# Performance work log

Measured on AMD Instinct MI355X. Metric: run time of the kernel, lower is better.

Reference implementation:

```python
import jax, jax.numpy as jnp
import numpy as np
from jax import lax

SEQ, IN, H, NC, L = 2048, 1024, 1024, 512, 3


def _lstm_layer(x_seq, W_ih, W_hh, b_ih, b_hh):
    # x_seq: [T, in] -> hs: [T, H]. PyTorch gate order: i, f, g, o.
    Hd = W_hh.shape[1]
    # Precompute input contribution for all timesteps (one big GEMM).
    gx = x_seq @ W_ih.T + (b_ih + b_hh)  # [T, 4H]

    def step(carry, gx_t):
        h, c = carry
        gates = gx_t + h @ W_hh.T  # [4H]
        i, f, g, o = jnp.split(gates, 4)
        i = jax.nn.sigmoid(i)
        f = jax.nn.sigmoid(f)
        g = jnp.tanh(g)
        o = jax.nn.sigmoid(o)
        c = f * c + i * g
        h = o * jnp.tanh(c)
        return (h, c), h

    h0 = jnp.zeros((Hd,), x_seq.dtype)
    c0 = jnp.zeros((Hd,), x_seq.dtype)
    _, hs = lax.scan(step, (h0, c0), gx)
    return hs


def setup_inputs() -> dict:
    key = jax.random.key(0)
    ks = jax.random.split(key, 16)
    s = 1.0 / np.sqrt(H)  # PyTorch LSTM init scale
    d = {"x": jax.random.normal(ks[0], (SEQ, IN), jnp.float32)}
    i = 1
    for l in range(L):
        in_dim = IN if l == 0 else H
        d[f"W_ih_{l}"] = jax.random.normal(ks[i], (4 * H, in_dim), jnp.float32) * s; i += 1
        d[f"W_hh_{l}"] = jax.random.normal(ks[i], (4 * H, H), jnp.float32) * s; i += 1
        d[f"b_ih_{l}"] = jax.random.normal(ks[i], (4 * H,), jnp.float32) * s; i += 1
        d[f"b_hh_{l}"] = jax.random.normal(ks[i], (4 * H,), jnp.float32) * s; i += 1
    d["fc_w"] = jax.random.normal(ks[13], (NC, H), jnp.float32) * s
    d["fc_b"] = jax.random.normal(ks[14], (NC,), jnp.float32) * s
    return d


def reference(x, W_ih_0, W_hh_0, b_ih_0, b_hh_0,
              W_ih_1, W_hh_1, b_ih_1, b_hh_1,
              W_ih_2, W_hh_2, b_ih_2, b_hh_2,
              fc_w, fc_b):
    h = _lstm_layer(x, W_ih_0, W_hh_0, b_ih_0, b_hh_0)
    h = _lstm_layer(h, W_ih_1, W_hh_1, b_ih_1, b_hh_1)
    h = _lstm_layer(h, W_ih_2, W_hh_2, b_ih_2, b_hh_2)
    return h @ fc_w.T + fc_b  # [SEQ, NC]
```

## Files before the change

kernel.cpp:

```cpp
#include <hip/hip_runtime.h>

#define HDIM  1024
#define FOURH 4096
#define TSEQ  2048
#define NCLS  512

#define SCANB  64
#define GEMMB  32
#define U16    16
#define DRING  128
#define GXRING 128
#define CHUNK  64
#define NCHUNK 32

#define CNT0 0
#define CNT1 64
#define CD0  128
#define CD1  192
#define SP1  256
#define SP2  320
#define SYNC_BYTES 2048
#define HDR_BYTES 32768

union SharedU {
    struct { float h[HDIM]; float gate[4][U16]; } scan;
    struct { float As[16][72]; float Bs[16][132]; } gemm;
};

__device__ __forceinline__ unsigned long long ald(const unsigned long long* p) {
    return __hip_atomic_load(p, __ATOMIC_RELAXED, __HIP_MEMORY_SCOPE_AGENT);
}
__device__ __forceinline__ void ast(unsigned long long* p, unsigned long long v) {
    __hip_atomic_store(p, v, __ATOMIC_RELAXED, __HIP_MEMORY_SCOPE_AGENT);
}
__device__ __forceinline__ unsigned ald32(const unsigned* p) {
    return __hip_atomic_load(p, __ATOMIC_RELAXED, __HIP_MEMORY_SCOPE_AGENT);
}
__device__ __forceinline__ void ast32(unsigned* p, unsigned v) {
    __hip_atomic_store(p, v, __ATOMIC_RELAXED, __HIP_MEMORY_SCOPE_AGENT);
}

__device__ __forceinline__ float fsig(float x)  { return 1.f / (1.f + __expf(-x)); }
__device__ __forceinline__ float ftanh(float x) { return 1.f - 2.f / (1.f + __expf(2.f * x)); }

__global__ __launch_bounds__(256) void gemm_bias_kernel(
    const float* __restrict__ A, const float* __restrict__ B,
    const float* __restrict__ bias1, const float* __restrict__ bias2,
    float* __restrict__ C, int M, int N, int K)
{
    __shared__ float As[16][68];
    __shared__ float Bs[16][68];

    const int tid = threadIdx.x;
    const int tx = tid & 15;
    const int ty = tid >> 4;
    const int n0 = blockIdx.x * 64;
    const int m0 = blockIdx.y * 64;
    const int r  = tid >> 2;
    const int kq = tid & 3;

    float acc[4][4];
#pragma unroll
    for (int i = 0; i < 4; ++i)
#pragma unroll
        for (int j = 0; j < 4; ++j) acc[i][j] = 0.f;

    for (int k0 = 0; k0 < K; k0 += 16) {
        float4 va = *(const float4*)&A[(size_t)(m0 + r) * K + k0 + 4 * kq];
        float4 vb = *(const float4*)&B[(size_t)(n0 + r) * K + k0 + 4 * kq];
        As[4 * kq + 0][r] = va.x; As[4 * kq + 1][r] = va.y;
        As[4 * kq + 2][r] = va.z; As[4 * kq + 3][r] = va.w;
        Bs[4 * kq + 0][r] = vb.x; Bs[4 * kq + 1][r] = vb.y;
        Bs[4 * kq + 2][r] = vb.z; Bs[4 * kq + 3][r] = vb.w;
        __syncthreads();
#pragma unroll
        for (int kk = 0; kk < 16; ++kk) {
            float4 a = *(const float4*)&As[kk][4 * ty];
            float4 b = *(const float4*)&Bs[kk][4 * tx];
            acc[0][0] = fmaf(a.x, b.x, acc[0][0]);
            acc[0][1] = fmaf(a.x, b.y, acc[0][1]);
            acc[0][2] = fmaf(a.x, b.z, acc[0][2]);
            acc[0][3] = fmaf(a.x, b.w, acc[0][3]);
            acc[1][0] = fmaf(a.y, b.x, acc[1][0]);
            acc[1][1] = fmaf(a.y, b.y, acc[1][1]);
            acc[1][2] = fmaf(a.y, b.z, acc[1][2]);
            acc[1][3] = fmaf(a.y, b.w, acc[1][3]);
            acc[2][0] = fmaf(a.z, b.x, acc[2][0]);
            acc[2][1] = fmaf(a.z, b.y, acc[2][1]);
            acc[2][2] = fmaf(a.z, b.z, acc[2][2]);
            acc[2][3] = fmaf(a.z, b.w, acc[2][3]);
            acc[3][0] = fmaf(a.w, b.x, acc[3][0]);
            acc[3][1] = fmaf(a.w, b.y, acc[3][1]);
            acc[3][2] = fmaf(a.w, b.z, acc[3][2]);
            acc[3][3] = fmaf(a.w, b.w, acc[3][3]);
        }
        __syncthreads();
    }

    float4 bv = *(const float4*)&bias1[n0 + 4 * tx];
    if (bias2) {
        float4 b2 = *(const float4*)&bias2[n0 + 4 * tx];
        bv.x += b2.x; bv.y += b2.y; bv.z += b2.z; bv.w += b2.w;
    }
#pragma unroll
    for (int i = 0; i < 4; ++i) {
        const int row = m0 + 4 * ty + i;
        float4 o;
        o.x = acc[i][0] + bv.x;
        o.y = acc[i][1] + bv.y;
        o.z = acc[i][2] + bv.z;
        o.w = acc[i][3] + bv.w;
        *(float4*)&C[(size_t)row * N + n0 + 4 * tx] = o;
    }
}

#define LOAD_GX(T) do { if (lane < 32) {                                      \
    const int g_ = lane >> 3, up_ = lane & 7;                                 \
    const unsigned long long pk_ = ald(gxb +                                  \
        (((size_t)((T) & gxmask)) * FOURH + g_ * HDIM + u0 + 2 * up_) / 2);   \
    gxlo = __uint_as_float((unsigned)pk_);                                    \
    gxhi = __uint_as_float((unsigned)(pk_ >> 32)); } } while (0)

__device__ void scan_role(int bi,
    const float* __restrict__ Whh,
    const unsigned long long* __restrict__ gxb, unsigned gxmask,
    unsigned long long* __restrict__ ring,
    const unsigned* cdSrc,
    const unsigned* cdBp,
    unsigned* sp,
    float* __restrict__ h2,
    SharedU* sm, unsigned* qflag)
{
    const int tid  = threadIdx.x;
    const int w    = tid >> 6;
    const int lane = tid & 63;
    const int g    = w & 3;
    const int ub   = (w >> 2) * 8;
    const int u0   = bi * U16;

    float4 wv[8][4];
#pragma unroll
    for (int u = 0; u < 8; ++u) {
        const float* Wr = Whh + (size_t)(g * HDIM + u0 + ub + u) * HDIM;
#pragma unroll
        for (int j = 0; j < 4; ++j)
            wv[u][j] = *(const float4*)(Wr + 256 * j + 4 * lane);
    }
    { float2 z = {0.f, 0.f}; *(float2*)(sm->scan.h + 2 * tid) = z; }
    if (tid < 4) qflag[tid] = 0u;
    float cst = 0.f;
    float gxlo = 0.f, gxhi = 0.f;
    __syncthreads();

    for (int t = 0; t < TSEQ; ++t) {
        if (w == 7) {
            if ((t & (CHUNK - 1)) == 0) {
                if (cdSrc && lane == 0) {
                    const unsigned need = (unsigned)(t >> 6) + 1u;
                    while (ald32(cdSrc) < need) __builtin_amdgcn_s_sleep(4);
                }
                LOAD_GX(t);
            }
            if (cdBp && t >= DRING && lane == 0) {
                const unsigned need = (unsigned)((t - DRING) >> 6) + 1u;
                while (ald32(cdBp) < need) __builtin_amdgcn_s_sleep(4);
            }
        }

        float acc[8];
#pragma unroll
        for (int u = 0; u < 8; ++u) acc[u] = 0.f;
#pragma unroll
        for (int j = 0; j < 4; ++j) {
            if (t) {
                const unsigned need = 2u * (unsigned)t;
                while (__hip_atomic_load(qflag + j, __ATOMIC_RELAXED,
                                         __HIP_MEMORY_SCOPE_WORKGROUP) < need) {}
                asm volatile("s_waitcnt lgkmcnt(0)" ::: "memory");
                __builtin_amdgcn_sched_barrier(0);
            }
            const float4 hvj = *(const float4*)(sm->scan.h + 256 * j + 4 * lane);
#pragma unroll
            for (int u = 0; u < 8; ++u) {
                acc[u] = fmaf(wv[u][j].x, hvj.x, acc[u]);
                acc[u] = fmaf(wv[u][j].y, hvj.y, acc[u]);
                acc[u] = fmaf(wv[u][j].z, hvj.z, acc[u]);
                acc[u] = fmaf(wv[u][j].w, hvj.w, acc[u]);
            }
        }
#pragma unroll
        for (int off = 32; off; off >>= 1)
#pragma unroll
            for (int u = 0; u < 8; ++u)
                acc[u] += __shfl_xor(acc[u], off, 64);
        if (lane == 0)
#pragma unroll
            for (int u = 0; u < 8; ++u) sm->scan.gate[g][ub + u] = acc[u];
        __syncthreads();

        const unsigned tag = (unsigned)(t + 1);
        if (w == 7) {
            const int src = (lane & 15) >> 1;
            float gv[4];
#pragma unroll
            for (int gg = 0; gg < 4; ++gg) {
                const float a = __shfl(gxlo, 8 * gg + src, 64);
                const float b = __shfl(gxhi, 8 * gg + src, 64);
                gv[gg] = (lane & 1) ? b : a;
            }
            if (lane < U16) {
                const float gi = sm->scan.gate[0][lane] + gv[0];
                const float gf = sm->scan.gate[1][lane] + gv[1];
                const float gg_ = sm->scan.gate[2][lane] + gv[2];
                const float go = sm->scan.gate[3][lane] + gv[3];
                const float si = fsig(gi);
                const float sf = fsig(gf);
                const float tg = ftanh(gg_);
                const float so = fsig(go);
                cst = sf * cst + si * tg;
                const float h = so * ftanh(cst);
                ast(ring + (size_t)(t & (DRING - 1)) * HDIM + u0 + lane,
                    ((unsigned long long)tag << 32) |
                    (unsigned long long)__float_as_uint(h));
                if (h2) h2[(size_t)t * HDIM + u0 + lane] = h;
            }
            if (sp && bi == 0 && lane == 0) ast32(sp, (unsigned)t);
            if (((t + 1) & (CHUNK - 1)) != 0 && t + 1 < TSEQ) LOAD_GX(t + 1);
        }

        if (t + 1 < TSEQ) {
            const unsigned long long* hb = ring + (size_t)(t & (DRING - 1)) * HDIM;
            unsigned long long v0 = 0, v1 = 0;
            bool got0 = false, got1 = false;
            while (!(got0 && got1)) {
                if (!got0) {
                    const unsigned long long x = ald(hb + 2 * tid);
                    if ((unsigned)(x >> 32) == tag) { v0 = x; got0 = true; }
                }
                if (!got1) {
                    const unsigned long long x = ald(hb + 2 * tid + 1);
                    if ((unsigned)(x >> 32) == tag) { v1 = x; got1 = true; }
                }
                if (!(got0 && got1)) __builtin_amdgcn_s_sleep(1);
            }
            sm->scan.h[2 * tid]     = __uint_as_float((unsigned)v0);
            sm->scan.h[2 * tid + 1] = __uint_as_float((unsigned)v1);
            asm volatile("s_waitcnt lgkmcnt(0)" ::: "memory");
            if (lane == 0)
                __hip_atomic_fetch_add(qflag + (w >> 1), 1u, __ATOMIC_RELAXED,
                                       __HIP_MEMORY_SCOPE_WORKGROUP);
        }
    }
}

__device__ void gemm_role(int tix,
    const unsigned long long* __restrict__ ringS,
    const float* __restrict__ Wih,
    const float* __restrict__ bih, const float* __restrict__ bhh,
    float* __restrict__ gxr,
    unsigned* cnt, unsigned* cd, const unsigned* spC,
    SharedU* sm)
{
    const int tid = threadIdx.x;
    const int tx = tid & 31, ty = tid >> 5;
    const int n0 = tix * 128;
    const int tt = tid >> 3, ke = tid & 7;
    const int cB = tid >> 2, kq = tid & 3;

    float4 bv;
    {
        const float4 b1 = *(const float4*)(bih + n0 + 4 * tx);
        const float4 b2 = *(const float4*)(bhh + n0 + 4 * tx);
        bv.x = b1.x + b2.x; bv.y = b1.y + b2.y;
        bv.z = b1.z + b2.z; bv.w = b1.w + b2.w;
    }
    unsigned long long* gxr64 = (unsigned long long*)gxr;

    for (int q = 0; q < NCHUNK; ++q) {
        if (q >= GXRING / CHUNK && tid == 0) {
            const unsigned need = (unsigned)((q - GXRING / CHUNK + 1) * CHUNK + 2);
            while (ald32(spC) < need) __builtin_amdgcn_s_sleep(8);
        }
        __syncthreads();

        float acc[4][4];
#pragma unroll
        for (int i = 0; i < 4; ++i)
#pragma unroll
            for (int j = 0; j < 4; ++j) acc[i][j] = 0.f;

        for (int k0 = 0; k0 < HDIM; k0 += 16) {
            {
                const int trow = q * CHUNK + tt;
                const unsigned expt = (unsigned)(trow + 1);
                const unsigned long long* srcp =
                    ringS + (size_t)(trow & (DRING - 1)) * HDIM + k0 + 2 * ke;
#pragma unroll
                for (int e = 0; e < 2; ++e) {
                    unsigned long long x;
                    while ((unsigned)((x = ald(srcp + e)) >> 32) != expt)
                        __builtin_amdgcn_s_sleep(1);
                    sm->gemm.As[2 * ke + e][tt] = __uint_as_float((unsigned)x);
                }
            }
            {
                const float4 vb = *(const float4*)(Wih + (size_t)(n0 + cB) * HDIM + k0 + 4 * kq);
                sm->gemm.Bs[4 * kq + 0][cB] = vb.x;
                sm->gemm.Bs[4 * kq + 1][cB] = vb.y;
                sm->gemm.Bs[4 * kq + 2][cB] = vb.z;
                sm->gemm.Bs[4 * kq + 3][cB] = vb.w;
            }
            __syncthreads();
#pragma unroll
            for (int kk = 0; kk < 16; ++kk) {
                const float4 a = *(const float4*)&sm->gemm.As[kk][4 * ty];
                const float4 b = *(const float4*)&sm->gemm.Bs[kk][4 * tx];
                acc[0][0] = fmaf(a.x, b.x, acc[0][0]);
                acc[0][1] = fmaf(a.x, b.y, acc[0][1]);
                acc[0][2] = fmaf(a.x, b.z, acc[0][2]);
                acc[0][3] = fmaf(a.x, b.w, acc[0][3]);
                acc[1][0] = fmaf(a.y, b.x, acc[1][0]);
                acc[1][1] = fmaf(a.y, b.y, acc[1][1]);
                acc[1][2] = fmaf(a.y, b.z, acc[1][2]);
                acc[1][3] = fmaf(a.y, b.w, acc[1][3]);
                acc[2][0] = fmaf(a.z, b.x, acc[2][0]);
                acc[2][1] = fmaf(a.z, b.y, acc[2][1]);
                acc[2][2] = fmaf(a.z, b.z, acc[2][2]);
                acc[2][3] = fmaf(a.z, b.w, acc[2][3]);
                acc[3][0] = fmaf(a.w, b.x, acc[3][0]);
                acc[3][1] = fmaf(a.w, b.y, acc[3][1]);
                acc[3][2] = fmaf(a.w, b.z, acc[3][2]);
                acc[3][3] = fmaf(a.w, b.w, acc[3][3]);
            }
            __syncthreads();
        }

#pragma unroll
        for (int i = 0; i < 4; ++i) {
            const int trow = q * CHUNK + 4 * ty + i;
            const float o0 = acc[i][0] + bv.x;
            const float o1 = acc[i][1] + bv.y;
            const float o2 = acc[i][2] + bv.z;
            const float o3 = acc[i][3] + bv.w;
            const size_t base =
                ((size_t)(trow & (GXRING - 1)) * FOURH + n0 + 4 * tx) / 2;
            ast(gxr64 + base,
                ((unsigned long long)__float_as_uint(o1) << 32) | __float_as_uint(o0));
            ast(gxr64 + base + 1,
                ((unsigned long long)__float_as_uint(o3) << 32) | __float_as_uint(o2));
        }
        asm volatile("s_waitcnt vmcnt(0)" ::: "memory");
        __syncthreads();
        if (tid == 0) {
            const unsigned old = __hip_atomic_fetch_add(cnt + q, 1u,
                                     __ATOMIC_RELAXED, __HIP_MEMORY_SCOPE_AGENT);
            if (old + 1u == (unsigned)GEMMB) ast32(cd, (unsigned)(q + 1));
        }
    }
}

__global__ __launch_bounds__(512) void fused_scan(
    const float* __restrict__ gx0,
    const float* __restrict__ Whh0, const float* __restrict__ Whh1,
    const float* __restrict__ Whh2,
    const float* __restrict__ Wih1, const float* __restrict__ Wih2,
    const float* __restrict__ bih1, const float* __restrict__ bhh1,
    const float* __restrict__ bih2, const float* __restrict__ bhh2,
    unsigned long long* ring0, unsigned long long* ring1, unsigned long long* ring2,
    float* gxr1, float* gxr2,
    float* h2out, unsigned* syncw)
{
    __shared__ SharedU sm;
    __shared__ unsigned qflag[4];
    const int lb = blockIdx.x;
    if (lb < 3 * SCANB) {
        const int layer = lb >> 6;
        const int bi    = lb & 63;
        if (layer == 0)
            scan_role(bi, Whh0, (const unsigned long long*)gx0, 2047u, ring0,
                      nullptr, syncw + CD0, nullptr, nullptr, &sm, qflag);
        else if (layer == 1)
            scan_role(bi, Whh1, (const unsigned long long*)gxr1, GXRING - 1u, ring1,
                      syncw + CD0, syncw + CD1, syncw + SP1, nullptr, &sm, qflag);
        else
            scan_role(bi, Whh2, (const unsigned long long*)gxr2, GXRING - 1u, ring2,
                      syncw + CD1, nullptr, syncw + SP2, h2out, &sm, qflag);
    } else {
        const int gb  = lb - 3 * SCANB;
        const int gl  = gb >> 5;
        const int tix = gb & 31;
        if (gl == 0)
            gemm_role(tix, ring0, Wih1, bih1, bhh1, gxr1,
                      syncw + CNT0, syncw + CD0, syncw + SP1, &sm);
        else
            gemm_role(tix, ring1, Wih2, bih2, bhh2, gxr2,
                      syncw + CNT1, syncw + CD1, syncw + SP2, &sm);
    }
}

extern "C" void kernel_launch(void* const* d_in, const int* in_sizes, int n_in,
                              void* d_out, int out_size, void* d_ws, size_t ws_size,
                              hipStream_t stream)
{
    (void)in_sizes; (void)n_in; (void)out_size; (void)ws_size;

    const float* x = (const float*)d_in[0];
    const float* W_ih[3] = {(const float*)d_in[1], (const float*)d_in[5], (const float*)d_in[9]};
    const float* W_hh[3] = {(const float*)d_in[2], (const float*)d_in[6], (const float*)d_in[10]};
    const float* b_ih[3] = {(const float*)d_in[3], (const float*)d_in[7], (const float*)d_in[11]};
    const float* b_hh[3] = {(const float*)d_in[4], (const float*)d_in[8], (const float*)d_in[12]};
    const float* fc_w = (const float*)d_in[13];
    const float* fc_b = (const float*)d_in[14];
    float* out = (float*)d_out;

    unsigned* syncw = (unsigned*)d_ws;
    float* gx = (float*)((char*)d_ws + HDR_BYTES);
    float* A  = gx + (size_t)TSEQ * FOURH;
    unsigned long long* ring0 = (unsigned long long*)(A + (size_t)TSEQ * HDIM);
    unsigned long long* ring1 = ring0 + (size_t)DRING * HDIM;
    unsigned long long* ring2 = ring1 + (size_t)DRING * HDIM;
    float* gxr1 = (float*)(ring2 + (size_t)DRING * HDIM);
    float* gxr2 = gxr1 + (size_t)GXRING * FOURH;

    hipMemsetAsync(syncw, 0, SYNC_BYTES, stream);

    {
        dim3 g(FOURH / 64, TSEQ / 64);
        gemm_bias_kernel<<<g, 256, 0, stream>>>(x, W_ih[0], b_ih[0], b_hh[0],
                                                gx, TSEQ, FOURH, HDIM);
    }

    {
        const float* gx0_c = gx;
        float* h2 = A;
        void* args[] = {
            (void*)&gx0_c,
            (void*)&W_hh[0], (void*)&W_hh[1], (void*)&W_hh[2],
            (void*)&W_ih[1], (void*)&W_ih[2],
            (void*)&b_ih[1], (void*)&b_hh[1],
            (void*)&b_ih[2], (void*)&b_hh[2],
            (void*)&ring0, (void*)&ring1, (void*)&ring2,
            (void*)&gxr1, (void*)&gxr2,
            (void*)&h2, (void*)&syncw
        };
        hipLaunchCooperativeKernel((void*)fused_scan,
                                   dim3(3 * SCANB + 2 * GEMMB), dim3(512),
                                   args, 0, stream);
    }

    {
        dim3 g(NCLS / 64, TSEQ / 64);
        gemm_bias_kernel<<<g, 256, 0, stream>>>(A, fc_w, fc_b, nullptr,
                                                out, TSEQ, NCLS, HDIM);
    }
}
```

Measured before the change: 8.066 ms.

## Distribute LSTM cell update across all waves and drop per-step block barrier

Each wave now owns two hidden units across all four gates, so the gate reduction and the cell update happen inside the wave instead of going through shared memory to a single wave. The per-step __syncthreads is replaced by a workgroup-scope atomic counter that guards the overwrite of shared h. The dot products use packed two-wide FMAs. This shortens the serial critical path of each recurrent step, at the cost of more complex shuffle reductions and a hand-built memory-ordering scheme that is delicate to get right.

```diff
diff --git a/kernel.cpp b/kernel.cpp
--- a/kernel.cpp
+++ b/kernel.cpp
@@ -22,8 +22,10 @@
 #define SYNC_BYTES 2048
 #define HDR_BYTES 32768
 
+typedef float v2f __attribute__((ext_vector_type(2)));
+
 union SharedU {
-    struct { float h[HDIM]; float gate[4][U16]; } scan;
+    struct { float h[HDIM]; } scan;
     struct { float As[16][72]; float Bs[16][132]; } gemm;
 };
 
@@ -114,12 +116,10 @@
     }
 }
 
-#define LOAD_GX(T) do { if (lane < 32) {                                      \
-    const int g_ = lane >> 3, up_ = lane & 7;                                 \
-    const unsigned long long pk_ = ald(gxb +                                  \
-        (((size_t)((T) & gxmask)) * FOURH + g_ * HDIM + u0 + 2 * up_) / 2);   \
-    gxlo = __uint_as_float((unsigned)pk_);                                    \
-    gxhi = __uint_as_float((unsigned)(pk_ >> 32)); } } while (0)
+#define LOAD_GXS(T) do { if (lane < 8) {                                      \
+    gxs = __uint_as_float(ald32((const unsigned*)gxb +                        \
+        (size_t)((T) & gxmask) * FOURH + (size_t)(lane >> 1) * HDIM           \
+        + u0 + 2 * w + (lane & 1))); } } while (0)
 
 __device__ void scan_role(int bi,
     const float* __restrict__ Whh,
@@ -129,47 +129,57 @@
     const unsigned* cdBp,
     unsigned* sp,
     float* __restrict__ h2,
-    SharedU* sm, unsigned* qflag)
+    SharedU* sm, unsigned* qflag, unsigned* rall)
 {
     const int tid  = threadIdx.x;
     const int w    = tid >> 6;
     const int lane = tid & 63;
-    const int g    = w & 3;
-    const int ub   = (w >> 2) * 8;
+    const int uu   = lane & 1;
     const int u0   = bi * U16;
 
-    float4 wv[8][4];
-#pragma unroll
-    for (int u = 0; u < 8; ++u) {
-        const float* Wr = Whh + (size_t)(g * HDIM + u0 + ub + u) * HDIM;
-#pragma unroll
-        for (int j = 0; j < 4; ++j)
-            wv[u][j] = *(const float4*)(Wr + 256 * j + 4 * lane);
+    v2f wv[8][8];
+#pragma unroll
+    for (int rg = 0; rg < 8; ++rg) {
+        const float* Wr = Whh +
+            (size_t)((rg >> 1) * HDIM + u0 + 2 * w + (rg & 1)) * HDIM;
+#pragma unroll
+        for (int j = 0; j < 4; ++j) {
+            const float4 q = *(const float4*)(Wr + 256 * j + 4 * lane);
+            v2f qa = {q.x, q.y}, qb = {q.z, q.w};
+            wv[rg][2 * j]     = qa;
+            wv[rg][2 * j + 1] = qb;
+        }
     }
     { float2 z = {0.f, 0.f}; *(float2*)(sm->scan.h + 2 * tid) = z; }
     if (tid < 4) qflag[tid] = 0u;
+    if (tid == 0) *rall = 0u;
     float cst = 0.f;
-    float gxlo = 0.f, gxhi = 0.f;
+    float gxs = 0.f;
+    unsigned cdc = 0u, bpc = 0u;
     __syncthreads();
 
     for (int t = 0; t < TSEQ; ++t) {
-        if (w == 7) {
-            if ((t & (CHUNK - 1)) == 0) {
-                if (cdSrc && lane == 0) {
-                    const unsigned need = (unsigned)(t >> 6) + 1u;
-                    while (ald32(cdSrc) < need) __builtin_amdgcn_s_sleep(4);
+        if (cdBp && t >= DRING && lane == 0) {
+            const unsigned need = (unsigned)((t - DRING) >> 6) + 1u;
+            while (bpc < need) {
+                bpc = ald32(cdBp);
+                if (bpc < need) __builtin_amdgcn_s_sleep(4);
+            }
+        }
+        if ((t & (CHUNK - 1)) == 0) {
+            if (cdSrc && lane == 0) {
+                const unsigned need = (unsigned)(t >> 6) + 1u;
+                while (cdc < need) {
+                    cdc = ald32(cdSrc);
+                    if (cdc < need) __builtin_amdgcn_s_sleep(4);
                 }
-                LOAD_GX(t);
-            }
-            if (cdBp && t >= DRING && lane == 0) {
-                const unsigned need = (unsigned)((t - DRING) >> 6) + 1u;
-                while (ald32(cdBp) < need) __builtin_amdgcn_s_sleep(4);
-            }
-        }
-
-        float acc[8];
-#pragma unroll
-        for (int u = 0; u < 8; ++u) acc[u] = 0.f;
+            }
+            LOAD_GXS(t);
+        }
+
+        v2f acc2[8];
+#pragma unroll
+        for (int rg = 0; rg < 8; ++rg) { v2f z = {0.f, 0.f}; acc2[rg] = z; }
 #pragma unroll
         for (int j = 0; j < 4; ++j) {
             if (t) {
@@ -179,54 +189,66 @@
                 asm volatile("s_waitcnt lgkmcnt(0)" ::: "memory");
                 __builtin_amdgcn_sched_barrier(0);
             }
-            const float4 hvj = *(const float4*)(sm->scan.h + 256 * j + 4 * lane);
-#pragma unroll
-            for (int u = 0; u < 8; ++u) {
-                acc[u] = fmaf(wv[u][j].x, hvj.x, acc[u]);
-                acc[u] = fmaf(wv[u][j].y, hvj.y, acc[u]);
-                acc[u] = fmaf(wv[u][j].z, hvj.z, acc[u]);
-                acc[u] = fmaf(wv[u][j].w, hvj.w, acc[u]);
-            }
-        }
-#pragma unroll
-        for (int off = 32; off; off >>= 1)
-#pragma unroll
-            for (int u = 0; u < 8; ++u)
-                acc[u] += __shfl_xor(acc[u], off, 64);
+            const float4 hq = *(const float4*)(sm->scan.h + 256 * j + 4 * lane);
+            const v2f hA = {hq.x, hq.y};
+            const v2f hB = {hq.z, hq.w};
+#pragma unroll
+            for (int rg = 0; rg < 8; ++rg) {
+                acc2[rg] = __builtin_elementwise_fma(wv[rg][2 * j],     hA, acc2[rg]);
+                acc2[rg] = __builtin_elementwise_fma(wv[rg][2 * j + 1], hB, acc2[rg]);
+            }
+        }
+        float a[8];
+#pragma unroll
+        for (int rg = 0; rg < 8; ++rg) a[rg] = acc2[rg].x + acc2[rg].y;
+
+        asm volatile("" ::: "memory");
         if (lane == 0)
-#pragma unroll
-            for (int u = 0; u < 8; ++u) sm->scan.gate[g][ub + u] = acc[u];
-        __syncthreads();
-
+            __hip_atomic_fetch_add(rall, 1u, __ATOMIC_RELAXED,
+                                   __HIP_MEMORY_SCOPE_WORKGROUP);
+
+#pragma unroll
+        for (int off = 1; off <= 4; off <<= 1)
+#pragma unroll
+            for (int rg = 0; rg < 8; ++rg)
+                a[rg] += __shfl_xor(a[rg], off, 64);
+        const int l7 = lane & 7;
+        const float s0 = (l7 & 1) ? a[1] : a[0];
+        const float s1 = (l7 & 1) ? a[3] : a[2];
+        const float s2 = (l7 & 1) ? a[5] : a[4];
+        const float s3 = (l7 & 1) ? a[7] : a[6];
+        const float t0 = (l7 & 2) ? s1 : s0;
+        const float t1 = (l7 & 2) ? s3 : s2;
+        float x = (l7 & 4) ? t1 : t0;
+        x += __shfl_xor(x, 8, 64);
+        x += __shfl_xor(x, 16, 64);
+        x += __shfl_xor(x, 32, 64);
+
+        float gsum[4], gxv[4];
+#pragma unroll
+        for (int g = 0; g < 4; ++g) {
+            gsum[g] = __shfl(x,   2 * g + uu, 64);
+            gxv[g]  = __shfl(gxs, 2 * g + uu, 64);
+        }
         const unsigned tag = (unsigned)(t + 1);
-        if (w == 7) {
-            const int src = (lane & 15) >> 1;
-            float gv[4];
-#pragma unroll
-            for (int gg = 0; gg < 4; ++gg) {
-                const float a = __shfl(gxlo, 8 * gg + src, 64);
-                const float b = __shfl(gxhi, 8 * gg + src, 64);
-                gv[gg] = (lane & 1) ? b : a;
-            }
-            if (lane < U16) {
-                const float gi = sm->scan.gate[0][lane] + gv[0];
-                const float gf = sm->scan.gate[1][lane] + gv[1];
-                const float gg_ = sm->scan.gate[2][lane] + gv[2];
-                const float go = sm->scan.gate[3][lane] + gv[3];
-                const float si = fsig(gi);
-                const float sf = fsig(gf);
-                const float tg = ftanh(gg_);
-                const float so = fsig(go);
-                cst = sf * cst + si * tg;
-                const float h = so * ftanh(cst);
-                ast(ring + (size_t)(t & (DRING - 1)) * HDIM + u0 + lane,
+        {
+            const float gi = gsum[0] + gxv[0];
+            const float gf = gsum[1] + gxv[1];
+            const float gg = gsum[2] + gxv[2];
+            const float go = gsum[3] + gxv[3];
+            const float si = fsig(gi), sf = fsig(gf);
+            const float tg = ftanh(gg), so = fsig(go);
+            cst = sf * cst + si * tg;
+            const float hval = so * ftanh(cst);
+            if (lane < 2) {
+                if (h2) h2[(size_t)t * HDIM + u0 + 2 * w + lane] = hval;
+                ast(ring + (size_t)(t & (DRING - 1)) * HDIM + u0 + 2 * w + lane,
                     ((unsigned long long)tag << 32) |
-                    (unsigned long long)__float_as_uint(h));
-                if (h2) h2[(size_t)t * HDIM + u0 + lane] = h;
-            }
-            if (sp && bi == 0 && lane == 0) ast32(sp, (unsigned)t);
-            if (((t + 1) & (CHUNK - 1)) != 0 && t + 1 < TSEQ) LOAD_GX(t + 1);
-        }
+                    (unsigned long long)__float_as_uint(hval));
+            }
+        }
+        if (sp && bi == 0 && w == 0 && lane == 0) ast32(sp, (unsigned)t);
+        if (((t + 1) & (CHUNK - 1)) != 0 && t + 1 < TSEQ) LOAD_GXS(t + 1);
 
         if (t + 1 < TSEQ) {
             const unsigned long long* hb = ring + (size_t)(t & (DRING - 1)) * HDIM;
@@ -234,18 +256,24 @@
             bool got0 = false, got1 = false;
             while (!(got0 && got1)) {
                 if (!got0) {
-                    const unsigned long long x = ald(hb + 2 * tid);
-                    if ((unsigned)(x >> 32) == tag) { v0 = x; got0 = true; }
+                    const unsigned long long y = ald(hb + 2 * tid);
+                    if ((unsigned)(y >> 32) == tag) { v0 = y; got0 = true; }
                 }
                 if (!got1) {
-                    const unsigned long long x = ald(hb + 2 * tid + 1);
-                    if ((unsigned)(x >> 32) == tag) { v1 = x; got1 = true; }
+                    const unsigned long long y = ald(hb + 2 * tid + 1);
+                    if ((unsigned)(y >> 32) == tag) { v1 = y; got1 = true; }
                 }
                 if (!(got0 && got1)) __builtin_amdgcn_s_sleep(1);
             }
+            const unsigned needR = 8u * (unsigned)(t + 1);
+            while (__hip_atomic_load(rall, __ATOMIC_RELAXED,
+                                     __HIP_MEMORY_SCOPE_WORKGROUP) < needR) {}
+            asm volatile("s_waitcnt lgkmcnt(0)" ::: "memory");
+            __builtin_amdgcn_sched_barrier(0);
             sm->scan.h[2 * tid]     = __uint_as_float((unsigned)v0);
             sm->scan.h[2 * tid + 1] = __uint_as_float((unsigned)v1);
             asm volatile("s_waitcnt lgkmcnt(0)" ::: "memory");
+            __builtin_amdgcn_sched_barrier(0);
             if (lane == 0)
                 __hip_atomic_fetch_add(qflag + (w >> 1), 1u, __ATOMIC_RELAXED,
                                        __HIP_MEMORY_SCOPE_WORKGROUP);
@@ -372,19 +400,20 @@
 {
     __shared__ SharedU sm;
     __shared__ unsigned qflag[4];
+    __shared__ unsigned rall;
     const int lb = blockIdx.x;
     if (lb < 3 * SCANB) {
         const int layer = lb >> 6;
         const int bi    = lb & 63;
         if (layer == 0)
             scan_role(bi, Whh0, (const unsigned long long*)gx0, 2047u, ring0,
-                      nullptr, syncw + CD0, nullptr, nullptr, &sm, qflag);
+                      nullptr, syncw + CD0, nullptr, nullptr, &sm, qflag, &rall);
         else if (layer == 1)
             scan_role(bi, Whh1, (const unsigned long long*)gxr1, GXRING - 1u, ring1,
-                      syncw + CD0, syncw + CD1, syncw + SP1, nullptr, &sm, qflag);
+                      syncw + CD0, syncw + CD1, syncw + SP1, nullptr, &sm, qflag, &rall);
         else
             scan_role(bi, Whh2, (const unsigned long long*)gxr2, GXRING - 1u, ring2,
-                      syncw + CD1, nullptr, syncw + SP2, h2out, &sm, qflag);
+                      syncw + CD1, nullptr, syncw + SP2, h2out, &sm, qflag, &rall);
     } else {
         const int gb  = lb - 3 * SCANB;
         const int gl  = gb >> 5;
```

New measurement: 9.951 ms. 23.4% more time.

## Gather h ring with a single wave and replace per-quarter flags with one flag

Applied to the files above, without the earlier changes.

Instead of all 8 waves each polling two tagged ring entries and bumping one of four quarter counters, wave 0 alone polls 16 contiguous entries per lane, writes them to shared memory as float4, and publishes a single step flag. Compute waves wait on that one flag, then load all four h chunks before doing the FMAs. Cross-block readiness counters are also cached in registers so they are not re-read once they are satisfied. The aim is to cut global polling traffic and intra-block sync overhead on the serial critical path. The cost is that the per-chunk overlap of compute with h arrival is lost and a single wave now serialises the gather.

```diff
diff --git a/kernel.cpp b/kernel.cpp
--- a/kernel.cpp
+++ b/kernel.cpp
@@ -129,7 +129,7 @@
     const unsigned* cdBp,
     unsigned* sp,
     float* __restrict__ h2,
-    SharedU* sm, unsigned* qflag)
+    SharedU* sm, unsigned* sflag)
 {
     const int tid  = threadIdx.x;
     const int w    = tid >> 6;
@@ -147,9 +147,10 @@
             wv[u][j] = *(const float4*)(Wr + 256 * j + 4 * lane);
     }
     { float2 z = {0.f, 0.f}; *(float2*)(sm->scan.h + 2 * tid) = z; }
-    if (tid < 4) qflag[tid] = 0u;
+    if (tid == 0) *sflag = 0u;
     float cst = 0.f;
     float gxlo = 0.f, gxhi = 0.f;
+    unsigned cdc = 0u, bpc = 0u;
     __syncthreads();
 
     for (int t = 0; t < TSEQ; ++t) {
@@ -157,36 +158,45 @@
             if ((t & (CHUNK - 1)) == 0) {
                 if (cdSrc && lane == 0) {
                     const unsigned need = (unsigned)(t >> 6) + 1u;
-                    while (ald32(cdSrc) < need) __builtin_amdgcn_s_sleep(4);
+                    while (cdc < need) {
+                        cdc = ald32(cdSrc);
+                        if (cdc < need) __builtin_amdgcn_s_sleep(4);
+                    }
                 }
                 LOAD_GX(t);
             }
             if (cdBp && t >= DRING && lane == 0) {
                 const unsigned need = (unsigned)((t - DRING) >> 6) + 1u;
-                while (ald32(cdBp) < need) __builtin_amdgcn_s_sleep(4);
-            }
-        }
-
+                while (bpc < need) {
+                    bpc = ald32(cdBp);
+                    if (bpc < need) __builtin_amdgcn_s_sleep(4);
+                }
+            }
+        }
+
+        if (t) {
+            while (__hip_atomic_load(sflag, __ATOMIC_RELAXED,
+                                     __HIP_MEMORY_SCOPE_WORKGROUP) < (unsigned)t) {}
+            asm volatile("s_waitcnt lgkmcnt(0)" ::: "memory");
+            __builtin_amdgcn_sched_barrier(0);
+        }
+
+        float4 hv[4];
+#pragma unroll
+        for (int j = 0; j < 4; ++j)
+            hv[j] = *(const float4*)(sm->scan.h + 256 * j + 4 * lane);
         float acc[8];
 #pragma unroll
-        for (int u = 0; u < 8; ++u) acc[u] = 0.f;
-#pragma unroll
-        for (int j = 0; j < 4; ++j) {
-            if (t) {
-                const unsigned need = 2u * (unsigned)t;
-                while (__hip_atomic_load(qflag + j, __ATOMIC_RELAXED,
-                                         __HIP_MEMORY_SCOPE_WORKGROUP) < need) {}
-                asm volatile("s_waitcnt lgkmcnt(0)" ::: "memory");
-                __builtin_amdgcn_sched_barrier(0);
-            }
-            const float4 hvj = *(const float4*)(sm->scan.h + 256 * j + 4 * lane);
-#pragma unroll
-            for (int u = 0; u < 8; ++u) {
-                acc[u] = fmaf(wv[u][j].x, hvj.x, acc[u]);
-                acc[u] = fmaf(wv[u][j].y, hvj.y, acc[u]);
-                acc[u] = fmaf(wv[u][j].z, hvj.z, acc[u]);
-                acc[u] = fmaf(wv[u][j].w, hvj.w, acc[u]);
-            }
+        for (int u = 0; u < 8; ++u) {
+            float a = 0.f;
+#pragma unroll
+            for (int j = 0; j < 4; ++j) {
+                a = fmaf(wv[u][j].x, hv[j].x, a);
+                a = fmaf(wv[u][j].y, hv[j].y, a);
+                a = fmaf(wv[u][j].z, hv[j].z, a);
+                a = fmaf(wv[u][j].w, hv[j].w, a);
+            }
+            acc[u] = a;
         }
 #pragma unroll
         for (int off = 32; off; off >>= 1)
@@ -228,27 +238,34 @@
             if (((t + 1) & (CHUNK - 1)) != 0 && t + 1 < TSEQ) LOAD_GX(t + 1);
         }
 
-        if (t + 1 < TSEQ) {
-            const unsigned long long* hb = ring + (size_t)(t & (DRING - 1)) * HDIM;
-            unsigned long long v0 = 0, v1 = 0;
-            bool got0 = false, got1 = false;
-            while (!(got0 && got1)) {
-                if (!got0) {
-                    const unsigned long long x = ald(hb + 2 * tid);
-                    if ((unsigned)(x >> 32) == tag) { v0 = x; got0 = true; }
-                }
-                if (!got1) {
-                    const unsigned long long x = ald(hb + 2 * tid + 1);
-                    if ((unsigned)(x >> 32) == tag) { v1 = x; got1 = true; }
-                }
-                if (!(got0 && got1)) __builtin_amdgcn_s_sleep(1);
-            }
-            sm->scan.h[2 * tid]     = __uint_as_float((unsigned)v0);
-            sm->scan.h[2 * tid + 1] = __uint_as_float((unsigned)v1);
+        if (w == 0 && t + 1 < TSEQ) {
+            const unsigned long long* hb =
+                ring + (size_t)(t & (DRING - 1)) * HDIM + 16 * lane;
+            unsigned long long y[16];
+            unsigned got = 0u;
+            do {
+#pragma unroll
+                for (int e = 0; e < 16; ++e)
+                    if (!(got & (1u << e))) y[e] = ald(hb + e);
+#pragma unroll
+                for (int e = 0; e < 16; ++e)
+                    if ((unsigned)(y[e] >> 32) == tag) got |= 1u << e;
+            } while (got != 0xFFFFu);
+            float* hd = sm->scan.h + 16 * lane;
+#pragma unroll
+            for (int k = 0; k < 4; ++k) {
+                float4 f;
+                f.x = __uint_as_float((unsigned)y[4 * k + 0]);
+                f.y = __uint_as_float((unsigned)y[4 * k + 1]);
+                f.z = __uint_as_float((unsigned)y[4 * k + 2]);
+                f.w = __uint_as_float((unsigned)y[4 * k + 3]);
+                *(float4*)(hd + 4 * k) = f;
+            }
             asm volatile("s_waitcnt lgkmcnt(0)" ::: "memory");
+            __builtin_amdgcn_sched_barrier(0);
             if (lane == 0)
-                __hip_atomic_fetch_add(qflag + (w >> 1), 1u, __ATOMIC_RELAXED,
-                                       __HIP_MEMORY_SCOPE_WORKGROUP);
+                __hip_atomic_store(sflag, tag, __ATOMIC_RELAXED,
+                                   __HIP_MEMORY_SCOPE_WORKGROUP);
         }
     }
 }
@@ -371,20 +388,20 @@
     float* h2out, unsigned* syncw)
 {
     __shared__ SharedU sm;
-    __shared__ unsigned qflag[4];
+    __shared__ unsigned sflag;
     const int lb = blockIdx.x;
     if (lb < 3 * SCANB) {
         const int layer = lb >> 6;
         const int bi    = lb & 63;
         if (layer == 0)
             scan_role(bi, Whh0, (const unsigned long long*)gx0, 2047u, ring0,
-                      nullptr, syncw + CD0, nullptr, nullptr, &sm, qflag);
+                      nullptr, syncw + CD0, nullptr, nullptr, &sm, &sflag);
         else if (layer == 1)
             scan_role(bi, Whh1, (const unsigned long long*)gxr1, GXRING - 1u, ring1,
-                      syncw + CD0, syncw + CD1, syncw + SP1, nullptr, &sm, qflag);
+                      syncw + CD0, syncw + CD1, syncw + SP1, nullptr, &sm, &sflag);
         else
             scan_role(bi, Whh2, (const unsigned long long*)gxr2, GXRING - 1u, ring2,
-                      syncw + CD1, nullptr, syncw + SP2, h2out, &sm, qflag);
+                      syncw + CD1, nullptr, syncw + SP2, h2out, &sm, &sflag);
     } else {
         const int gb  = lb - 3 * SCANB;
         const int gl  = gb >> 5;
```

Result: slower. 11.47 ms (+42.2%).
